# Performance work log

Hardware: AMD Instinct MI355X
Metric: run time of the kernel (lower is better)

Reference implementation:

```python
import jax, jax.numpy as jnp
import numpy as np

HID = 1024      # hidden_dim (== input_dim, forced by spectral feedback)
LAYERS = 3      # num_layers
OUT = 2500      # output_dim = 50*50
GRID = 50       # spatial grid side
MODES = 32      # kept Fourier modes per side


def setup_inputs() -> dict:
    key = jax.random.key(0)
    ks = jax.random.split(key, 7)
    B = 32
    s = 0.02  # small init so tanh/sigmoid stay in a sane range over 64 steps
    return {
        "x": jax.random.normal(ks[0], (B, 1, HID), jnp.float32),
        "W_ih": jax.random.normal(ks[1], (LAYERS, 3 * HID, HID), jnp.float32) * s,
        "W_hh": jax.random.normal(ks[2], (LAYERS, 3 * HID, HID), jnp.float32) * s,
        "b_ih": jax.random.normal(ks[3], (LAYERS, 3 * HID), jnp.float32) * s,
        "b_hh": jax.random.normal(ks[4], (LAYERS, 3 * HID), jnp.float32) * s,
        "fc_w": jax.random.normal(ks[5], (OUT, HID), jnp.float32) * s,
        "fc_b": jax.random.normal(ks[6], (OUT,), jnp.float32) * s,
        "time_size": 64,
    }


def _gru_cell(x, h, w_ih, w_hh, b_ih, b_hh):
    # PyTorch GRU cell: r,z,n gate ordering in the stacked 3H weight matrices.
    gi = x @ w_ih.T + b_ih            # (B, 3H)
    gh = h @ w_hh.T + b_hh            # (B, 3H)
    i_r, i_z, i_n = jnp.split(gi, 3, axis=-1)
    h_r, h_z, h_n = jnp.split(gh, 3, axis=-1)
    r = jax.nn.sigmoid(i_r + h_r)
    z = jax.nn.sigmoid(i_z + h_z)
    n = jnp.tanh(i_n + r * h_n)
    return (1.0 - z) * n + z * h


def _spectral_crop(out):
    # out: (B, 1, OUT) -> real(fftn) -> fftshift -> center 32x32 crop -> (B,1,1024)
    B = out.shape[0]
    sq = out.reshape(B, 1, GRID, GRID)
    f = jnp.real(jnp.fft.fftn(sq, axes=(2, 3)))
    f = jnp.fft.fftshift(f, axes=(2, 3))
    lo = GRID // 2 - MODES // 2   # 9
    hi = GRID // 2 + MODES // 2   # 41
    return f[:, :, lo:hi, lo:hi].astype(jnp.float32).reshape(B, 1, MODES * MODES)


def reference(x, W_ih, W_hh, b_ih, b_hh, fc_w, fc_b, time_size):
    B = x.shape[0]
    h0 = jnp.zeros((LAYERS, B, HID), x.dtype)

    def step(carry, _):
        xin, h = carry
        inp = xin[:, 0, :]                         # seq len is 1: (B, HID)
        hs = []
        for l in range(LAYERS):                    # fixed small layer loop
            hl = _gru_cell(inp, h[l], W_ih[l], W_hh[l], b_ih[l], b_hh[l])
            hs.append(hl)
            inp = hl
        h_new = jnp.stack(hs, axis=0)              # (LAYERS, B, HID)
        out = (inp @ fc_w.T + fc_b)[:, None, :]    # (B, 1, OUT)
        x_next = _spectral_crop(out)               # (B, 1, HID) spectral feedback
        return (x_next, h_new), out

    (_, _), outputs = jax.lax.scan(step, (x, h0), None, length=int(time_size))
    return outputs  # (time_size, B, 1, OUT)
```

## Files before the change

### kernel.cpp

```cpp
#include <hip/hip_runtime.h>
#include <hip/hip_bf16.h>

typedef __attribute__((ext_vector_type(8))) short bf16x8;
typedef __attribute__((ext_vector_type(4))) float f32x4;

#define HID 1024
#define BATCH 32
#define NACT (BATCH * HID)
#define NWIH (3 * 3 * HID * HID)
#define LSTRIDE (3 * HID * HID)
#define NFC (2500 * HID)
#define WXN (HID * HID)
#define G3 (3 * HID)
#define TSTEPS 64
#define NBLK 256
#define NTHR 512
#define FSTRIDE 32

__device__ __forceinline__ f32x4 mfma16(bf16x8 a, bf16x8 b, f32x4 c) {
  return __builtin_amdgcn_mfma_f32_16x16x32_bf16(a, b, c, 0, 0, 0);
}
__device__ __forceinline__ float bfbits2f(unsigned short u) {
  return __uint_as_float(((unsigned int)u) << 16);
}
__device__ __forceinline__ unsigned short f2bf_rn(float v) {
  union { __hip_bfloat16 b; unsigned short s; } cv;
  cv.b = __float2bfloat16(v);
  return cv.s;
}
__device__ __forceinline__ void split3(float v, unsigned short& s0, unsigned short& s1,
                                       unsigned short& s2) {
  s0 = (unsigned short)(__float_as_uint(v) >> 16);
  float r1 = v - bfbits2f(s0);
  s1 = (unsigned short)(__float_as_uint(r1) >> 16);
  float r2 = r1 - bfbits2f(s1);
  s2 = f2bf_rn(r2);
}
__device__ __forceinline__ void split2(float v, unsigned short& s0, unsigned short& s1) {
  s0 = (unsigned short)(__float_as_uint(v) >> 16);
  s1 = f2bf_rn(v - bfbits2f(s0));
}
__device__ __forceinline__ bf16x8 ld_act16(const unsigned short* p) {
  union { unsigned long long u[2]; bf16x8 v; } cv;
  cv.u[0] = __hip_atomic_load((unsigned long long*)p, __ATOMIC_RELAXED, __HIP_MEMORY_SCOPE_AGENT);
  cv.u[1] = __hip_atomic_load((unsigned long long*)p + 1, __ATOMIC_RELAXED, __HIP_MEMORY_SCOPE_AGENT);
  return cv.v;
}
__device__ __forceinline__ float ld_f32(const float* p) {
  return __hip_atomic_load(p, __ATOMIC_RELAXED, __HIP_MEMORY_SCOPE_AGENT);
}
__device__ __forceinline__ void st_f32(float* p, float v) {
  __hip_atomic_store(p, v, __ATOMIC_RELAXED, __HIP_MEMORY_SCOPE_AGENT);
}
__device__ __forceinline__ void pst_plane(unsigned short* plane, int eidx, unsigned short s,
                                          int par) {
  int other = __shfl_xor((int)(unsigned int)s, 1, 64);
  unsigned int packed = ((unsigned int)s) | (((unsigned int)(unsigned short)other) << 16);
  if (!par)
    __hip_atomic_store((unsigned int*)(plane + eidx), packed, __ATOMIC_RELAXED,
                       __HIP_MEMORY_SCOPE_AGENT);
}

__global__ void convert_weights(const float* __restrict__ Wih, const float* __restrict__ Whh,
                                const float* __restrict__ fcw, unsigned short* __restrict__ WIHP,
                                unsigned short* __restrict__ WHHP, unsigned short* __restrict__ FCWP) {
  int i0 = blockIdx.x * blockDim.x + threadIdx.x;
  int st = gridDim.x * blockDim.x;
  for (int i = i0; i < NWIH; i += st) {
    unsigned short a0, a1, a2, b0, b1, b2;
    split3(Wih[i], a0, a1, a2);
    split3(Whh[i], b0, b1, b2);
    WIHP[i] = a0; WIHP[NWIH + i] = a1; WIHP[2 * NWIH + i] = a2;
    WHHP[i] = b0; WHHP[NWIH + i] = b1; WHHP[2 * NWIH + i] = b2;
  }
  for (int i = i0; i < NFC; i += st) {
    unsigned short c0, c1;
    split2(fcw[i], c0, c1);
    FCWP[i] = c0; FCWP[NFC + i] = c1;
  }
}

__global__ void k_trig(float* __restrict__ cA, float* __restrict__ sA) {
  int i = blockIdx.x * blockDim.x + threadIdx.x;
  if (i < 32 * 50) {
    int a = i / 50, n = i % 50;
    int ka = (a + 34) % 50;
    int ph = (ka * n) % 50;
    float ang = 6.283185307179586f * (float)ph / 50.0f;
    cA[i] = cosf(ang);
    sA[i] = sinf(ang);
  }
}

__global__ void k_pq(const float* __restrict__ fcw, const float* __restrict__ cA,
                     const float* __restrict__ sA, float* __restrict__ P, float* __restrict__ Q,
                     int k0) {
  int n1 = blockIdx.x / 2;
  int kk = (blockIdx.x & 1) * 256 + threadIdx.x;
  int k = k0 + kk;
  float accP[32], accQ[32];
#pragma unroll
  for (int c = 0; c < 32; ++c) { accP[c] = 0.f; accQ[c] = 0.f; }
  for (int n2 = 0; n2 < 50; ++n2) {
    float w = fcw[(n1 * 50 + n2) * HID + k];
#pragma unroll
    for (int c = 0; c < 32; ++c) {
      accP[c] = fmaf(w, cA[c * 50 + n2], accP[c]);
      accQ[c] = fmaf(w, sA[c * 50 + n2], accQ[c]);
    }
  }
#pragma unroll
  for (int c = 0; c < 32; ++c) {
    P[(n1 * 32 + c) * 512 + kk] = accP[c];
    Q[(n1 * 32 + c) * 512 + kk] = accQ[c];
  }
}

__global__ void k_wx(const float* __restrict__ P, const float* __restrict__ Q,
                     const float* __restrict__ cA, const float* __restrict__ sA,
                     unsigned short* __restrict__ WXP, int k0) {
  int j = blockIdx.x;
  int a = j >> 5, c = j & 31;
  float acc[2] = {0.f, 0.f};
  for (int n1 = 0; n1 < 50; ++n1) {
    float ca = cA[a * 50 + n1], sa = sA[a * 50 + n1];
    int base = (n1 * 32 + c) * 512;
#pragma unroll
    for (int i = 0; i < 2; ++i) {
      int kk = threadIdx.x + 256 * i;
      acc[i] = fmaf(ca, P[base + kk], acc[i]);
      acc[i] = fmaf(-sa, Q[base + kk], acc[i]);
    }
  }
#pragma unroll
  for (int i = 0; i < 2; ++i) {
    int kk = threadIdx.x + 256 * i;
    unsigned short s0, s1, s2;
    split3(acc[i], s0, s1, s2);
    int idx = j * HID + k0 + kk;
    WXP[idx] = s0;
    WXP[WXN + idx] = s1;
    WXP[2 * WXN + idx] = s2;
  }
}

__global__ void k_cx(const float* __restrict__ fcb, const float* __restrict__ cA,
                     const float* __restrict__ sA, float* __restrict__ CXV) {
  int j = blockIdx.x * blockDim.x + threadIdx.x;
  if (j >= HID) return;
  int a = j >> 5, c = j & 31;
  float acc = 0.f;
  for (int n1 = 0; n1 < 50; ++n1)
    for (int n2 = 0; n2 < 50; ++n2)
      acc += fcb[n1 * 50 + n2] * (cA[a * 50 + n1] * cA[c * 50 + n2] - sA[a * 50 + n1] * sA[c * 50 + n2]);
  CXV[j] = acc;
}

__global__ void setup_state(const float* __restrict__ x_in, float* __restrict__ H,
                            unsigned short* __restrict__ HBP, unsigned short* __restrict__ XBP,
                            unsigned int* __restrict__ flags, unsigned int* __restrict__ rel) {
  int i0 = blockIdx.x * blockDim.x + threadIdx.x;
  int st = gridDim.x * blockDim.x;
  for (int k = i0; k < NBLK * FSTRIDE; k += st) flags[k] = 0u;
  if (i0 == 0) *rel = 0u;
  for (int k = i0; k < 3 * NACT; k += st) H[k] = 0.0f;
  for (int k = i0; k < 3 * 3 * NACT; k += st) HBP[k] = 0;
  for (int k = i0; k < NACT; k += st) {
    unsigned short s0, s1, s2;
    split3(x_in[k], s0, s1, s2);
    XBP[k] = s0; XBP[NACT + k] = s1; XBP[2 * NACT + k] = s2;
  }
}

__device__ __forceinline__ void gbar(unsigned int* flags, unsigned int* rel, unsigned int e) {
  __syncthreads();
  const int tid = threadIdx.x;
  const int bid = blockIdx.x;
  if (tid == 0)
    __hip_atomic_store(flags + bid * FSTRIDE, e, __ATOMIC_RELAXED, __HIP_MEMORY_SCOPE_AGENT);
  if (bid == 0) {
    if (tid < 64) {
      for (;;) {
        bool ok = true;
#pragma unroll
        for (int i = 0; i < 4; ++i) {
          unsigned int v = __hip_atomic_load(flags + (tid + 64 * i) * FSTRIDE, __ATOMIC_RELAXED,
                                             __HIP_MEMORY_SCOPE_AGENT);
          ok &= (v >= e);
        }
        if (__all(ok)) break;
        __builtin_amdgcn_s_sleep(1);
      }
      if (tid == 0)
        __hip_atomic_store(rel, e, __ATOMIC_RELAXED, __HIP_MEMORY_SCOPE_AGENT);
    }
  } else if (tid == 0) {
    while (__hip_atomic_load(rel, __ATOMIC_RELAXED, __HIP_MEMORY_SCOPE_AGENT) < e)
      __builtin_amdgcn_s_sleep(1);
  }
  __syncthreads();
}

__device__ __forceinline__ void gemm_reduce(const unsigned short* __restrict__ Bp, long bplane,
                                            const unsigned short* __restrict__ Ap, int gfbase,
                                            float* smem, f32x4 acc[2]) {
  const int tid = threadIdx.x;
  const int L = tid & 63, w = tid >> 6;
  const int col = L & 15, quad = L >> 4;
  acc[0] = {0.f, 0.f, 0.f, 0.f};
  acc[1] = {0.f, 0.f, 0.f, 0.f};
  const unsigned short* brow = Bp + (size_t)(gfbase + col) * HID;
  for (int it = 0; it < 4; ++it) {
    int k0 = w * 128 + it * 32 + quad * 8;
    bf16x8 a[3][2], b[3];
#pragma unroll
    for (int mh = 0; mh < 2; ++mh) {
      int r = (mh * 16 + col) * HID + k0;
#pragma unroll
      for (int p = 0; p < 3; ++p) a[p][mh] = ld_act16(Ap + (size_t)p * NACT + r);
    }
#pragma unroll
    for (int p = 0; p < 3; ++p) b[p] = *(const bf16x8*)(brow + (size_t)p * bplane + k0);
#pragma unroll
    for (int p = 0; p < 3; ++p)
#pragma unroll
      for (int q = 0; q < 3 - p; ++q)
#pragma unroll
        for (int mh = 0; mh < 2; ++mh) acc[mh] = mfma16(a[p][mh], b[q], acc[mh]);
  }
  __syncthreads();
  if (w > 0) {
    float* s = smem + ((w - 1) * 64 + L) * 8;
    *(f32x4*)s = acc[0];
    *(f32x4*)(s + 4) = acc[1];
  }
  __syncthreads();
  if (w == 0) {
#pragma unroll
    for (int s = 0; s < 7; ++s) {
      const float* p = smem + ((s * 64) + L) * 8;
      acc[0] += *(const f32x4*)p;
      acc[1] += *(const f32x4*)(p + 4);
    }
  }
}

__global__ __launch_bounds__(NTHR, 2) void rnn_persistent(
    const unsigned short* __restrict__ WIHP, const unsigned short* __restrict__ WHHP,
    const unsigned short* __restrict__ WXP,
    const float* __restrict__ b_ih, const float* __restrict__ b_hh, const float* __restrict__ CXV,
    float* __restrict__ H,
    unsigned short* __restrict__ HBP,
    unsigned short* __restrict__ XBP,
    float* __restrict__ GH,
    float* __restrict__ GI,
    unsigned short* __restrict__ HIST0, unsigned short* __restrict__ HIST1,
    unsigned int* __restrict__ FLAGS, unsigned int* __restrict__ REL) {
  __shared__ float smem[3584];
  const int tid = threadIdx.x;
  const int L = tid & 63, w = tid >> 6;
  const int col = L & 15, quad = L >> 4;
  const int bid = blockIdx.x;
  unsigned int ep = 0;

#pragma unroll 1
  for (int t = 0; t < TSTEPS; ++t) {
#pragma unroll 1
    for (int i = 0; i < 3; ++i) {
      int tau = bid + NBLK * i;
      int s = tau / 192, tile = tau % 192;
      int gf = tile * 16;
      const unsigned short* Bp;
      const unsigned short* Ap;
      float* outp;
      if (s < 3) {
        Bp = WHHP + (size_t)s * LSTRIDE;
        Ap = HBP + (size_t)s * 3 * NACT;
        outp = GH + (size_t)s * (32 * G3);
      } else {
        Bp = WIHP;
        Ap = XBP;
        outp = GI;
      }
      f32x4 acc[2];
      gemm_reduce(Bp, NWIH, Ap, gf, smem, acc);
      if (w == 0) {
#pragma unroll
        for (int mh = 0; mh < 2; ++mh)
#pragma unroll
          for (int r = 0; r < 4; ++r) {
            int b = mh * 16 + quad * 4 + r;
            st_f32(outp + (size_t)b * G3 + gf + col, acc[mh][r]);
          }
      }
    }
    gbar(FLAGS, REL, ++ep);

#pragma unroll 1
    for (int l = 0; l < 3; ++l) {
      if (bid < 64) {
        int jt = bid * 16;
        int b = tid >> 4, jj = tid & 15, j = jt + jj;
        float gi[3], gh[3];
#pragma unroll
        for (int g = 0; g < 3; ++g) {
          gi[g] = ld_f32(GI + (size_t)b * G3 + g * HID + j);
          gh[g] = ld_f32(GH + (size_t)l * (32 * G3) + (size_t)b * G3 + g * HID + j);
        }
        float ir = gi[0] + b_ih[l * G3 + j];
        float iz = gi[1] + b_ih[l * G3 + HID + j];
        float in_ = gi[2] + b_ih[l * G3 + 2 * HID + j];
        float hr = gh[0] + b_hh[l * G3 + j];
        float hz = gh[1] + b_hh[l * G3 + HID + j];
        float hn = gh[2] + b_hh[l * G3 + 2 * HID + j];
        float rr = 1.0f / (1.0f + expf(-(ir + hr)));
        float zz = 1.0f / (1.0f + expf(-(iz + hz)));
        float nn = tanhf(in_ + rr * hn);
        float hold = H[(size_t)l * NACT + b * HID + j];
        float hnew = (1.0f - zz) * nn + zz * hold;
        H[(size_t)l * NACT + b * HID + j] = hnew;
        unsigned short s0, s1, s2;
        split3(hnew, s0, s1, s2);
        int eidx = b * HID + j;
        unsigned short* hb = HBP + (size_t)l * 3 * NACT;
        int par = tid & 1;
        pst_plane(hb, eidx, s0, par);
        pst_plane(hb + NACT, eidx, s1, par);
        pst_plane(hb + 2 * NACT, eidx, s2, par);
        if (l == 2) {
          HIST0[(size_t)(t * BATCH + b) * HID + j] = s0;
          HIST1[(size_t)(t * BATCH + b) * HID + j] = s1;
        }
      }
      gbar(FLAGS, REL, ++ep);

      if (l < 2) {
        if (bid < 192) {
          int gf = bid * 16;
          f32x4 acc[2];
          gemm_reduce(WIHP + (size_t)(l + 1) * LSTRIDE, NWIH, HBP + (size_t)l * 3 * NACT, gf,
                      smem, acc);
          if (w == 0) {
#pragma unroll
            for (int mh = 0; mh < 2; ++mh)
#pragma unroll
              for (int r = 0; r < 4; ++r) {
                int b = mh * 16 + quad * 4 + r;
                st_f32(GI + (size_t)b * G3 + gf + col, acc[mh][r]);
              }
          }
        }
        gbar(FLAGS, REL, ++ep);
      }
    }

    if (t < TSTEPS - 1) {
      if (bid < 64) {
        int jt = bid * 16;
        f32x4 acc[2];
        gemm_reduce(WXP, WXN, HBP + (size_t)2 * 3 * NACT, jt, smem, acc);
        if (w == 0) {
          int j = jt + col;
          float cx = CXV[j];
          int par = col & 1;
#pragma unroll
          for (int mh = 0; mh < 2; ++mh)
#pragma unroll
            for (int r = 0; r < 4; ++r) {
              int b = mh * 16 + quad * 4 + r;
              float xv = acc[mh][r] + cx;
              unsigned short s0, s1, s2;
              split3(xv, s0, s1, s2);
              int eidx = b * HID + j;
              pst_plane(XBP, eidx, s0, par);
              pst_plane(XBP + NACT, eidx, s1, par);
              pst_plane(XBP + 2 * NACT, eidx, s2, par);
            }
        }
      }
      gbar(FLAGS, REL, ++ep);
    }
  }
}

__global__ __launch_bounds__(256) void final_fc(const unsigned short* __restrict__ H0,
                                                const unsigned short* __restrict__ H1,
                                                const unsigned short* __restrict__ FCWP,
                                                const float* __restrict__ fcb,
                                                float* __restrict__ dout) {
  int tid = threadIdx.x;
  int L = tid & 63, ws = tid >> 6;
  int col = L & 15, quad = L >> 4;
  int m0 = blockIdx.y * 64 + ws * 16;
  int jt = blockIdx.x * 64;
  f32x4 acc[4];
#pragma unroll
  for (int s = 0; s < 4; ++s) acc[s] = {0.f, 0.f, 0.f, 0.f};
  for (int kt = 0; kt < 32; ++kt) {
    int k0 = kt * 32 + quad * 8;
    bf16x8 ah = *(const bf16x8*)(H0 + (size_t)(m0 + col) * HID + k0);
    bf16x8 am = *(const bf16x8*)(H1 + (size_t)(m0 + col) * HID + k0);
    bf16x8 bh[4], bm[4];
#pragma unroll
    for (int s = 0; s < 4; ++s) {
      int jr = jt + s * 16 + col;
      int rc = jr < 2500 ? jr : 2499;
      bh[s] = *(const bf16x8*)(FCWP + (size_t)rc * HID + k0);
      bm[s] = *(const bf16x8*)(FCWP + (size_t)NFC + (size_t)rc * HID + k0);
    }
#pragma unroll
    for (int s = 0; s < 4; ++s) {
      acc[s] = mfma16(ah, bh[s], acc[s]);
      acc[s] = mfma16(ah, bm[s], acc[s]);
      acc[s] = mfma16(am, bh[s], acc[s]);
    }
  }
#pragma unroll
  for (int s = 0; s < 4; ++s) {
    int j = jt + s * 16 + col;
    if (j < 2500) {
      float bias = fcb[j];
#pragma unroll
      for (int r = 0; r < 4; ++r) {
        int R = m0 + quad * 4 + r;
        dout[(size_t)R * 2500 + j] = acc[s][r] + bias;
      }
    }
  }
}

extern "C" void kernel_launch(void* const* d_in, const int* in_sizes, int n_in,
                              void* d_out, int out_size, void* d_ws, size_t ws_size,
                              hipStream_t stream) {
  const float* x_in = (const float*)d_in[0];
  const float* W_ih = (const float*)d_in[1];
  const float* W_hh = (const float*)d_in[2];
  const float* b_ih = (const float*)d_in[3];
  const float* b_hh = (const float*)d_in[4];
  const float* fc_w = (const float*)d_in[5];
  const float* fc_b = (const float*)d_in[6];
  float* dout = (float*)d_out;
  char* ws = (char*)d_ws;

  unsigned short* WIHP = (unsigned short*)(ws + 0);
  unsigned short* WHHP = (unsigned short*)(ws + 56623104);
  unsigned short* FCWP = (unsigned short*)(ws + 113246208);
  unsigned short* WXP  = (unsigned short*)(ws + 123486208);
  float* H             = (float*)(ws + 129777664);
  unsigned short* HBP  = (unsigned short*)(ws + 130170880);
  unsigned short* XBP  = (unsigned short*)(ws + 130760704);
  float* GH            = (float*)(ws + 130957312);
  float* GI            = (float*)(ws + 132136960);
  float* CXV           = (float*)(ws + 132530176);
  float* CA            = (float*)(ws + 132534272);
  float* SA            = (float*)(ws + 132540672);
  unsigned short* HIST0 = (unsigned short*)(ws + 132547328);
  unsigned short* HIST1 = (unsigned short*)(ws + 136741632);
  unsigned int* FLAGS  = (unsigned int*)(ws + 140935936);
  unsigned int* REL    = (unsigned int*)(ws + 140968704);
  float* Pbuf          = (float*)(ws + 132547328);
  float* Qbuf          = (float*)(ws + 135824128);

  k_trig<<<7, 256, 0, stream>>>(CA, SA);
  for (int k0 = 0; k0 < 1024; k0 += 512) {
    k_pq<<<100, 256, 0, stream>>>(fc_w, CA, SA, Pbuf, Qbuf, k0);
    k_wx<<<1024, 256, 0, stream>>>(Pbuf, Qbuf, CA, SA, WXP, k0);
  }
  k_cx<<<4, 256, 0, stream>>>(fc_b, CA, SA, CXV);
  convert_weights<<<2048, 256, 0, stream>>>(W_ih, W_hh, fc_w, WIHP, WHHP, FCWP);
  setup_state<<<512, 256, 0, stream>>>(x_in, H, HBP, XBP, FLAGS, REL);
  rnn_persistent<<<NBLK, NTHR, 0, stream>>>(WIHP, WHHP, WXP, b_ih, b_hh, CXV, H, HBP, XBP,
                                            GH, GI, HIST0, HIST1, FLAGS, REL);
  final_fc<<<dim3(40, 32), 256, 0, stream>>>(HIST0, HIST1, FCWP, fc_b, dout);
}
```

Measured before the change: 6.899 ms.

## Fold spectral feedback into layer-0 input weights and drop per-step feedback phase

Precomputes a composed matrix W_ih0·Wx (Fourier crop map) with an MFMA GEMM and a folded bias b_ih0 + W_ih0·cx. Layer-0 input gates are then computed directly from the last layer's hidden state in the same phase as the recurrent GEMMs. This removes the separate feedback GEMM and one grid barrier per timestep. The per-step phase is also retiled to 48 columns per block across all 256 blocks, and workspace reuse is reorganised (fc_w conversion moved after the RNN). It adds one-off setup work and changes numerical precision: the composed weights are stored as a 2-way bf16 split instead of 3-way.

Result: faster. 5.706 ms (-17.3%).

```diff
diff --git a/kernel.cpp b/kernel.cpp
--- a/kernel.cpp
+++ b/kernel.cpp
@@ -11,6 +11,7 @@
 #define LSTRIDE (3 * HID * HID)
 #define NFC (2500 * HID)
 #define WXN (HID * HID)
+#define WXIN (3 * HID * HID)
 #define G3 (3 * HID)
 #define TSTEPS 64
 #define NBLK 256
@@ -62,8 +63,7 @@
 }
 
 __global__ void convert_weights(const float* __restrict__ Wih, const float* __restrict__ Whh,
-                                const float* __restrict__ fcw, unsigned short* __restrict__ WIHP,
-                                unsigned short* __restrict__ WHHP, unsigned short* __restrict__ FCWP) {
+                                unsigned short* __restrict__ WIHP, unsigned short* __restrict__ WHHP) {
   int i0 = blockIdx.x * blockDim.x + threadIdx.x;
   int st = gridDim.x * blockDim.x;
   for (int i = i0; i < NWIH; i += st) {
@@ -73,6 +73,11 @@
     WIHP[i] = a0; WIHP[NWIH + i] = a1; WIHP[2 * NWIH + i] = a2;
     WHHP[i] = b0; WHHP[NWIH + i] = b1; WHHP[2 * NWIH + i] = b2;
   }
+}
+
+__global__ void convert_fcw(const float* __restrict__ fcw, unsigned short* __restrict__ FCWP) {
+  int i0 = blockIdx.x * blockDim.x + threadIdx.x;
+  int st = gridDim.x * blockDim.x;
   for (int i = i0; i < NFC; i += st) {
     unsigned short c0, c1;
     split2(fcw[i], c0, c1);
@@ -95,8 +100,8 @@
 __global__ void k_pq(const float* __restrict__ fcw, const float* __restrict__ cA,
                      const float* __restrict__ sA, float* __restrict__ P, float* __restrict__ Q,
                      int k0) {
-  int n1 = blockIdx.x / 2;
-  int kk = (blockIdx.x & 1) * 256 + threadIdx.x;
+  int n1 = blockIdx.x;
+  int kk = threadIdx.x;
   int k = k0 + kk;
   float accP[32], accQ[32];
 #pragma unroll
@@ -111,36 +116,84 @@
   }
 #pragma unroll
   for (int c = 0; c < 32; ++c) {
-    P[(n1 * 32 + c) * 512 + kk] = accP[c];
-    Q[(n1 * 32 + c) * 512 + kk] = accQ[c];
+    P[(n1 * 32 + c) * 256 + kk] = accP[c];
+    Q[(n1 * 32 + c) * 256 + kk] = accQ[c];
   }
 }
 
 __global__ void k_wx(const float* __restrict__ P, const float* __restrict__ Q,
                      const float* __restrict__ cA, const float* __restrict__ sA,
-                     unsigned short* __restrict__ WXP, int k0) {
+                     float* __restrict__ WxF, int k0) {
   int j = blockIdx.x;
   int a = j >> 5, c = j & 31;
-  float acc[2] = {0.f, 0.f};
+  int kk = threadIdx.x;
+  float acc = 0.f;
   for (int n1 = 0; n1 < 50; ++n1) {
-    float ca = cA[a * 50 + n1], sa = sA[a * 50 + n1];
-    int base = (n1 * 32 + c) * 512;
-#pragma unroll
-    for (int i = 0; i < 2; ++i) {
-      int kk = threadIdx.x + 256 * i;
-      acc[i] = fmaf(ca, P[base + kk], acc[i]);
-      acc[i] = fmaf(-sa, Q[base + kk], acc[i]);
-    }
-  }
-#pragma unroll
-  for (int i = 0; i < 2; ++i) {
-    int kk = threadIdx.x + 256 * i;
+    int base = (n1 * 32 + c) * 256 + kk;
+    acc = fmaf(cA[a * 50 + n1], P[base], acc);
+    acc = fmaf(-sA[a * 50 + n1], Q[base], acc);
+  }
+  WxF[j * HID + k0 + kk] = acc;
+}
+
+__global__ void k_transpose(const float* __restrict__ WxF, unsigned short* __restrict__ WXTP) {
+  __shared__ float lds[64][65];
+  int f0 = blockIdx.x * 64, h0 = blockIdx.y * 64;
+  for (int idx = threadIdx.x; idx < 4096; idx += 256) {
+    int r = idx >> 6, c = idx & 63;
+    lds[r][c] = WxF[(f0 + r) * HID + h0 + c];
+  }
+  __syncthreads();
+  for (int idx = threadIdx.x; idx < 4096; idx += 256) {
+    int r = idx >> 6, c = idx & 63;
     unsigned short s0, s1, s2;
-    split3(acc[i], s0, s1, s2);
-    int idx = j * HID + k0 + kk;
-    WXP[idx] = s0;
-    WXP[WXN + idx] = s1;
-    WXP[2 * WXN + idx] = s2;
+    split3(lds[c][r], s0, s1, s2);
+    int o = (h0 + r) * HID + f0 + c;
+    WXTP[o] = s0; WXTP[WXN + o] = s1; WXTP[2 * WXN + o] = s2;
+  }
+}
+
+__global__ __launch_bounds__(256) void k_compose(const unsigned short* __restrict__ WIHP,
+                                                 const unsigned short* __restrict__ WXTP,
+                                                 unsigned short* __restrict__ WXIP) {
+  int tid = threadIdx.x;
+  int L = tid & 63, ws = tid >> 6;
+  int col = L & 15, quad = L >> 4;
+  int m0 = blockIdx.y * 64 + ws * 16;
+  int jt = blockIdx.x * 64;
+  f32x4 acc[4];
+#pragma unroll
+  for (int s = 0; s < 4; ++s) acc[s] = {0.f, 0.f, 0.f, 0.f};
+  for (int kt = 0; kt < 32; ++kt) {
+    int k0 = kt * 32 + quad * 8;
+    bf16x8 a[3], b[3][4];
+#pragma unroll
+    for (int p = 0; p < 3; ++p)
+      a[p] = *(const bf16x8*)(WIHP + (size_t)p * NWIH + (m0 + col) * HID + k0);
+#pragma unroll
+    for (int s = 0; s < 4; ++s)
+#pragma unroll
+      for (int p = 0; p < 3; ++p)
+        b[p][s] = *(const bf16x8*)(WXTP + (size_t)p * WXN + (jt + s * 16 + col) * HID + k0);
+#pragma unroll
+    for (int p = 0; p < 3; ++p)
+#pragma unroll
+      for (int q = 0; q < 3; ++q)
+        if (p + q <= 2)
+#pragma unroll
+          for (int s = 0; s < 4; ++s) acc[s] = mfma16(a[q], b[p][s], acc[s]);
+  }
+#pragma unroll
+  for (int s = 0; s < 4; ++s) {
+    int h = jt + s * 16 + col;
+#pragma unroll
+    for (int r = 0; r < 4; ++r) {
+      int g = m0 + quad * 4 + r;
+      unsigned short s0, s1;
+      split2(acc[s][r], s0, s1);
+      WXIP[(size_t)g * HID + h] = s0;
+      WXIP[(size_t)WXIN + (size_t)g * HID + h] = s1;
+    }
   }
 }
 
@@ -154,6 +207,21 @@
     for (int n2 = 0; n2 < 50; ++n2)
       acc += fcb[n1 * 50 + n2] * (cA[a * 50 + n1] * cA[c * 50 + n2] - sA[a * 50 + n1] * sA[c * 50 + n2]);
   CXV[j] = acc;
+}
+
+__global__ void k_bih0c(const float* __restrict__ b_ih, const float* __restrict__ CXV,
+                        const float* __restrict__ Wih, float* __restrict__ BIH0C) {
+  __shared__ float red[256];
+  int g = blockIdx.x;
+  float p = 0.f;
+  for (int k = threadIdx.x; k < HID; k += 256) p = fmaf(CXV[k], Wih[(size_t)g * HID + k], p);
+  red[threadIdx.x] = p;
+  __syncthreads();
+  for (int s = 128; s > 0; s >>= 1) {
+    if (threadIdx.x < s) red[threadIdx.x] += red[threadIdx.x + s];
+    __syncthreads();
+  }
+  if (threadIdx.x == 0) BIH0C[g] = b_ih[g] + red[0];
 }
 
 __global__ void setup_state(const float* __restrict__ x_in, float* __restrict__ H,
@@ -191,8 +259,7 @@
         if (__all(ok)) break;
         __builtin_amdgcn_s_sleep(1);
       }
-      if (tid == 0)
-        __hip_atomic_store(rel, e, __ATOMIC_RELAXED, __HIP_MEMORY_SCOPE_AGENT);
+      if (tid == 0) __hip_atomic_store(rel, e, __ATOMIC_RELAXED, __HIP_MEMORY_SCOPE_AGENT);
     }
   } else if (tid == 0) {
     while (__hip_atomic_load(rel, __ATOMIC_RELAXED, __HIP_MEMORY_SCOPE_AGENT) < e)
@@ -201,62 +268,99 @@
   __syncthreads();
 }
 
-__device__ __forceinline__ void gemm_reduce(const unsigned short* __restrict__ Bp, long bplane,
-                                            const unsigned short* __restrict__ Ap, int gfbase,
-                                            float* smem, f32x4 acc[2]) {
+template <int NWP, int NT>
+__device__ __forceinline__ void gemm_nt(const unsigned short* __restrict__ Bp, size_t bplane,
+                                        const unsigned short* __restrict__ Ap, int gfbase,
+                                        float* smem, f32x4 (&acc)[NT][2]) {
   const int tid = threadIdx.x;
   const int L = tid & 63, w = tid >> 6;
   const int col = L & 15, quad = L >> 4;
-  acc[0] = {0.f, 0.f, 0.f, 0.f};
-  acc[1] = {0.f, 0.f, 0.f, 0.f};
-  const unsigned short* brow = Bp + (size_t)(gfbase + col) * HID;
+#pragma unroll
+  for (int n = 0; n < NT; ++n) {
+    acc[n][0] = {0.f, 0.f, 0.f, 0.f};
+    acc[n][1] = {0.f, 0.f, 0.f, 0.f};
+  }
   for (int it = 0; it < 4; ++it) {
     int k0 = w * 128 + it * 32 + quad * 8;
-    bf16x8 a[3][2], b[3];
+    bf16x8 a[3][2], b[NWP][NT];
 #pragma unroll
     for (int mh = 0; mh < 2; ++mh) {
       int r = (mh * 16 + col) * HID + k0;
 #pragma unroll
-      for (int p = 0; p < 3; ++p) a[p][mh] = ld_act16(Ap + (size_t)p * NACT + r);
-    }
-#pragma unroll
-    for (int p = 0; p < 3; ++p) b[p] = *(const bf16x8*)(brow + (size_t)p * bplane + k0);
-#pragma unroll
-    for (int p = 0; p < 3; ++p)
-#pragma unroll
-      for (int q = 0; q < 3 - p; ++q)
-#pragma unroll
-        for (int mh = 0; mh < 2; ++mh) acc[mh] = mfma16(a[p][mh], b[q], acc[mh]);
+      for (int q = 0; q < 3; ++q) a[q][mh] = ld_act16(Ap + (size_t)q * NACT + r);
+    }
+#pragma unroll
+    for (int n = 0; n < NT; ++n) {
+      int rr = (gfbase + n * 16 + col) * HID + k0;
+#pragma unroll
+      for (int p = 0; p < NWP; ++p) b[p][n] = *(const bf16x8*)(Bp + (size_t)p * bplane + rr);
+    }
+#pragma unroll
+    for (int p = 0; p < NWP; ++p)
+#pragma unroll
+      for (int q = 0; q < 3; ++q)
+        if (p + q <= 2)
+#pragma unroll
+          for (int n = 0; n < NT; ++n)
+#pragma unroll
+            for (int mh = 0; mh < 2; ++mh) acc[n][mh] = mfma16(a[q][mh], b[p][n], acc[n][mh]);
   }
   __syncthreads();
   if (w > 0) {
-    float* s = smem + ((w - 1) * 64 + L) * 8;
-    *(f32x4*)s = acc[0];
-    *(f32x4*)(s + 4) = acc[1];
+    float* s = smem + ((w - 1) * 64 + L) * (NT * 8);
+#pragma unroll
+    for (int n = 0; n < NT; ++n) {
+      *(f32x4*)(s + n * 8) = acc[n][0];
+      *(f32x4*)(s + n * 8 + 4) = acc[n][1];
+    }
   }
   __syncthreads();
   if (w == 0) {
 #pragma unroll
-    for (int s = 0; s < 7; ++s) {
-      const float* p = smem + ((s * 64) + L) * 8;
-      acc[0] += *(const f32x4*)p;
-      acc[1] += *(const f32x4*)(p + 4);
-    }
+    for (int sx = 0; sx < 7; ++sx) {
+      const float* p = smem + (sx * 64 + L) * (NT * 8);
+#pragma unroll
+      for (int n = 0; n < NT; ++n) {
+        acc[n][0] += *(const f32x4*)(p + n * 8);
+        acc[n][1] += *(const f32x4*)(p + n * 8 + 4);
+      }
+    }
+  }
+}
+
+__global__ __launch_bounds__(NTHR, 2) void gi0_first(const unsigned short* __restrict__ WIHP,
+                                                     const unsigned short* __restrict__ XBP,
+                                                     float* __restrict__ GI) {
+  __shared__ float smem[3584];
+  const int tid = threadIdx.x;
+  const int L = tid & 63, w = tid >> 6;
+  const int col = L & 15, quad = L >> 4;
+  int gf = blockIdx.x * 16;
+  f32x4 acc[1][2];
+  gemm_nt<3, 1>(WIHP, NWIH, XBP, gf, smem, acc);
+  if (w == 0) {
+#pragma unroll
+    for (int mh = 0; mh < 2; ++mh)
+#pragma unroll
+      for (int r = 0; r < 4; ++r) {
+        int b = mh * 16 + quad * 4 + r;
+        st_f32(GI + (size_t)b * G3 + gf + col, acc[0][mh][r]);
+      }
   }
 }
 
 __global__ __launch_bounds__(NTHR, 2) void rnn_persistent(
     const unsigned short* __restrict__ WIHP, const unsigned short* __restrict__ WHHP,
-    const unsigned short* __restrict__ WXP,
-    const float* __restrict__ b_ih, const float* __restrict__ b_hh, const float* __restrict__ CXV,
+    const unsigned short* __restrict__ WXIP,
+    const float* __restrict__ b_ih, const float* __restrict__ b_hh,
+    const float* __restrict__ BIH0C,
     float* __restrict__ H,
     unsigned short* __restrict__ HBP,
-    unsigned short* __restrict__ XBP,
     float* __restrict__ GH,
     float* __restrict__ GI,
     unsigned short* __restrict__ HIST0, unsigned short* __restrict__ HIST1,
     unsigned int* __restrict__ FLAGS, unsigned int* __restrict__ REL) {
-  __shared__ float smem[3584];
+  __shared__ float smem[10752];
   const int tid = threadIdx.x;
   const int L = tid & 63, w = tid >> 6;
   const int col = L & 15, quad = L >> 4;
@@ -265,33 +369,38 @@
 
 #pragma unroll 1
   for (int t = 0; t < TSTEPS; ++t) {
-#pragma unroll 1
-    for (int i = 0; i < 3; ++i) {
-      int tau = bid + NBLK * i;
-      int s = tau / 192, tile = tau % 192;
-      int gf = tile * 16;
-      const unsigned short* Bp;
-      const unsigned short* Ap;
-      float* outp;
+    {
+      int s = bid >> 6;
+      int gf = (bid & 63) * 48;
       if (s < 3) {
-        Bp = WHHP + (size_t)s * LSTRIDE;
-        Ap = HBP + (size_t)s * 3 * NACT;
-        outp = GH + (size_t)s * (32 * G3);
-      } else {
-        Bp = WIHP;
-        Ap = XBP;
-        outp = GI;
-      }
-      f32x4 acc[2];
-      gemm_reduce(Bp, NWIH, Ap, gf, smem, acc);
-      if (w == 0) {
-#pragma unroll
-        for (int mh = 0; mh < 2; ++mh)
-#pragma unroll
-          for (int r = 0; r < 4; ++r) {
-            int b = mh * 16 + quad * 4 + r;
-            st_f32(outp + (size_t)b * G3 + gf + col, acc[mh][r]);
-          }
+        f32x4 acc[3][2];
+        gemm_nt<3, 3>(WHHP + (size_t)s * LSTRIDE, NWIH, HBP + (size_t)s * 3 * NACT, gf, smem, acc);
+        if (w == 0) {
+          float* outp = GH + (size_t)s * (32 * G3);
+#pragma unroll
+          for (int n = 0; n < 3; ++n)
+#pragma unroll
+            for (int mh = 0; mh < 2; ++mh)
+#pragma unroll
+              for (int r = 0; r < 4; ++r) {
+                int b = mh * 16 + quad * 4 + r;
+                st_f32(outp + (size_t)b * G3 + gf + n * 16 + col, acc[n][mh][r]);
+              }
+        }
+      } else if (t > 0) {
+        f32x4 acc[3][2];
+        gemm_nt<2, 3>(WXIP, WXIN, HBP + (size_t)2 * 3 * NACT, gf, smem, acc);
+        if (w == 0) {
+#pragma unroll
+          for (int n = 0; n < 3; ++n)
+#pragma unroll
+            for (int mh = 0; mh < 2; ++mh)
+#pragma unroll
+              for (int r = 0; r < 4; ++r) {
+                int b = mh * 16 + quad * 4 + r;
+                st_f32(GI + (size_t)b * G3 + gf + n * 16 + col, acc[n][mh][r]);
+              }
+        }
       }
     }
     gbar(FLAGS, REL, ++ep);
@@ -301,18 +410,20 @@
       if (bid < 64) {
         int jt = bid * 16;
         int b = tid >> 4, jj = tid & 15, j = jt + jj;
+        const float* bi_base = (l == 0) ? ((t == 0) ? b_ih : BIH0C) : (b_ih + l * G3);
+        const float* bh_base = b_hh + l * G3;
         float gi[3], gh[3];
 #pragma unroll
         for (int g = 0; g < 3; ++g) {
           gi[g] = ld_f32(GI + (size_t)b * G3 + g * HID + j);
           gh[g] = ld_f32(GH + (size_t)l * (32 * G3) + (size_t)b * G3 + g * HID + j);
         }
-        float ir = gi[0] + b_ih[l * G3 + j];
-        float iz = gi[1] + b_ih[l * G3 + HID + j];
-        float in_ = gi[2] + b_ih[l * G3 + 2 * HID + j];
-        float hr = gh[0] + b_hh[l * G3 + j];
-        float hz = gh[1] + b_hh[l * G3 + HID + j];
-        float hn = gh[2] + b_hh[l * G3 + 2 * HID + j];
+        float ir = gi[0] + bi_base[j];
+        float iz = gi[1] + bi_base[HID + j];
+        float in_ = gi[2] + bi_base[2 * HID + j];
+        float hr = gh[0] + bh_base[j];
+        float hz = gh[1] + bh_base[HID + j];
+        float hn = gh[2] + bh_base[2 * HID + j];
         float rr = 1.0f / (1.0f + expf(-(ir + hr)));
         float zz = 1.0f / (1.0f + expf(-(iz + hz)));
         float nn = tanhf(in_ + rr * hn);
@@ -337,48 +448,21 @@
       if (l < 2) {
         if (bid < 192) {
           int gf = bid * 16;
-          f32x4 acc[2];
-          gemm_reduce(WIHP + (size_t)(l + 1) * LSTRIDE, NWIH, HBP + (size_t)l * 3 * NACT, gf,
-                      smem, acc);
+          f32x4 acc[1][2];
+          gemm_nt<3, 1>(WIHP + (size_t)(l + 1) * LSTRIDE, NWIH, HBP + (size_t)l * 3 * NACT, gf,
+                        smem, acc);
           if (w == 0) {
 #pragma unroll
             for (int mh = 0; mh < 2; ++mh)
 #pragma unroll
               for (int r = 0; r < 4; ++r) {
                 int b = mh * 16 + quad * 4 + r;
-                st_f32(GI + (size_t)b * G3 + gf + col, acc[mh][r]);
+                st_f32(GI + (size_t)b * G3 + gf + col, acc[0][mh][r]);
               }
           }
         }
         gbar(FLAGS, REL, ++ep);
       }
-    }
-
-    if (t < TSTEPS - 1) {
-      if (bid < 64) {
-        int jt = bid * 16;
-        f32x4 acc[2];
-        gemm_reduce(WXP, WXN, HBP + (size_t)2 * 3 * NACT, jt, smem, acc);
-        if (w == 0) {
-          int j = jt + col;
-          float cx = CXV[j];
-          int par = col & 1;
-#pragma unroll
-          for (int mh = 0; mh < 2; ++mh)
-#pragma unroll
-            for (int r = 0; r < 4; ++r) {
-              int b = mh * 16 + quad * 4 + r;
-              float xv = acc[mh][r] + cx;
-              unsigned short s0, s1, s2;
-              split3(xv, s0, s1, s2);
-              int eidx = b * HID + j;
-              pst_plane(XBP, eidx, s0, par);
-              pst_plane(XBP + NACT, eidx, s1, par);
-              pst_plane(XBP + 2 * NACT, eidx, s2, par);
-            }
-        }
-      }
-      gbar(FLAGS, REL, ++ep);
     }
   }
 }
@@ -444,32 +528,40 @@
 
   unsigned short* WIHP = (unsigned short*)(ws + 0);
   unsigned short* WHHP = (unsigned short*)(ws + 56623104);
+  unsigned short* WXIP = (unsigned short*)(ws + 113246208);
   unsigned short* FCWP = (unsigned short*)(ws + 113246208);
-  unsigned short* WXP  = (unsigned short*)(ws + 123486208);
-  float* H             = (float*)(ws + 129777664);
-  unsigned short* HBP  = (unsigned short*)(ws + 130170880);
-  unsigned short* XBP  = (unsigned short*)(ws + 130760704);
-  float* GH            = (float*)(ws + 130957312);
-  float* GI            = (float*)(ws + 132136960);
-  float* CXV           = (float*)(ws + 132530176);
-  float* CA            = (float*)(ws + 132534272);
-  float* SA            = (float*)(ws + 132540672);
-  unsigned short* HIST0 = (unsigned short*)(ws + 132547328);
-  unsigned short* HIST1 = (unsigned short*)(ws + 136741632);
-  unsigned int* FLAGS  = (unsigned int*)(ws + 140935936);
-  unsigned int* REL    = (unsigned int*)(ws + 140968704);
-  float* Pbuf          = (float*)(ws + 132547328);
-  float* Qbuf          = (float*)(ws + 135824128);
+  float* Pbuf          = (float*)(ws + 125829120);
+  float* Qbuf          = (float*)(ws + 127467520);
+  float* WxF           = (float*)(ws + 129105920);
+  unsigned short* WXTP = (unsigned short*)(ws + 133300224);
+  unsigned short* HIST0 = (unsigned short*)(ws + 125829120);
+  unsigned short* HIST1 = (unsigned short*)(ws + 130023424);
+  float* H             = (float*)(ws + 139591680);
+  unsigned short* HBP  = (unsigned short*)(ws + 139984896);
+  unsigned short* XBP  = (unsigned short*)(ws + 140574720);
+  float* GH            = (float*)(ws + 140771328);
+  float* GI            = (float*)(ws + 141950976);
+  float* CXV           = (float*)(ws + 142344192);
+  float* CA            = (float*)(ws + 142348288);
+  float* SA            = (float*)(ws + 142354688);
+  float* BIH0C         = (float*)(ws + 142361088);
+  unsigned int* FLAGS  = (unsigned int*)(ws + 142373376);
+  unsigned int* REL    = (unsigned int*)(ws + 142406144);
 
   k_trig<<<7, 256, 0, stream>>>(CA, SA);
-  for (int k0 = 0; k0 < 1024; k0 += 512) {
-    k_pq<<<100, 256, 0, stream>>>(fc_w, CA, SA, Pbuf, Qbuf, k0);
-    k_wx<<<1024, 256, 0, stream>>>(Pbuf, Qbuf, CA, SA, WXP, k0);
-  }
+  for (int k0 = 0; k0 < 1024; k0 += 256) {
+    k_pq<<<50, 256, 0, stream>>>(fc_w, CA, SA, Pbuf, Qbuf, k0);
+    k_wx<<<1024, 256, 0, stream>>>(Pbuf, Qbuf, CA, SA, WxF, k0);
+  }
+  k_transpose<<<dim3(16, 16), 256, 0, stream>>>(WxF, WXTP);
+  convert_weights<<<2048, 256, 0, stream>>>(W_ih, W_hh, WIHP, WHHP);
+  k_compose<<<dim3(16, 48), 256, 0, stream>>>(WIHP, WXTP, WXIP);
   k_cx<<<4, 256, 0, stream>>>(fc_b, CA, SA, CXV);
-  convert_weights<<<2048, 256, 0, stream>>>(W_ih, W_hh, fc_w, WIHP, WHHP, FCWP);
+  k_bih0c<<<3072, 256, 0, stream>>>(b_ih, CXV, W_ih, BIH0C);
   setup_state<<<512, 256, 0, stream>>>(x_in, H, HBP, XBP, FLAGS, REL);
-  rnn_persistent<<<NBLK, NTHR, 0, stream>>>(WIHP, WHHP, WXP, b_ih, b_hh, CXV, H, HBP, XBP,
+  gi0_first<<<192, NTHR, 0, stream>>>(WIHP, XBP, GI);
+  rnn_persistent<<<NBLK, NTHR, 0, stream>>>(WIHP, WHHP, WXIP, b_ih, b_hh, BIH0C, H, HBP,
                                             GH, GI, HIST0, HIST1, FLAGS, REL);
+  convert_fcw<<<1024, 256, 0, stream>>>(fc_w, FCWP);
   final_fc<<<dim3(40, 32), 256, 0, stream>>>(HIST0, HIST1, FCWP, fc_b, dout);
 }
```
